# Optimization experiments

Hardware: AMD Instinct MI355X
Metric: run time of the kernel (lower is better)

Reference implementation:

```python
import jax, jax.numpy as jnp
import numpy as np

B, N = 4, 2048
K_GLOBAL, K_LOCAL = 32, 16
EMB, OUT_C = 1024, 40
NEG, EPS = 0.2, 1e-5


def _bn(x, p, axis=1):
    # p: (4, C) stacked (gamma, beta, running_mean, running_var); eval-mode BN
    g, b, m, v = p
    sh = [1] * x.ndim
    sh[axis] = -1
    return (x - m.reshape(sh)) * (g.reshape(sh) * jax.lax.rsqrt(v.reshape(sh) + EPS)) + b.reshape(sh)


def _knn(geod, allow, k):
    # geod: (B,N,N) affinity (larger = closer, as in DGCNN's -dist^2 convention)
    # allow: (B,N) bool columns that may be selected
    mn = jnp.min(geod, axis=-1, keepdims=True)           # (B,N,1) row minima
    pd = jnp.where(allow[:, None, :], geod, mn)          # disallowed cols -> row min (never picked)
    return jax.lax.top_k(pd, k)[1]                       # (B,N,k)


def _edge_conv(x, geod, allow, k, w, bnp):
    # x: (B,C,N); EdgeConv: gather neighbors, cat(nbr-ctr, ctr), 1x1 conv, BN, LeakyReLU, max over k
    idx = _knn(geod, allow, k)                           # (B,N,k)
    xt = jnp.swapaxes(x, 1, 2)                           # (B,N,C)
    nbr = jax.vmap(lambda a, i: a[i])(xt, idx)           # (B,N,k,C)
    ctr = xt[:, :, None, :]
    feat = jnp.concatenate([nbr - ctr, jnp.broadcast_to(ctr, nbr.shape)], axis=-1)  # (B,N,k,2C)
    y = jnp.einsum('oc,bnkc->bonk', w, feat)             # 1x1 conv (no bias)
    y = jax.nn.leaky_relu(_bn(y, bnp, 1), NEG)
    return jnp.max(y, axis=-1)                           # (B,O,N)


def setup_inputs() -> dict:
    key = jax.random.key(0)
    ks = list(jax.random.split(key, 64))
    it = iter(ks)
    d = {}
    d['x'] = jax.random.normal(next(it), (B, 3, N), jnp.float32)
    d['local_idx'] = jax.random.randint(next(it), (B, N), 0, 2).astype(bool)
    d['geod_dist'] = jax.random.normal(next(it), (B, N, N), jnp.float32)
    dims = [(64, 6), (64, 128), (128, 128), (256, 256), (64, 6), (64, 128), (128, 128), (256, 256), (EMB, 512)]
    for i, (o, c) in enumerate(dims, 1):
        d[f'w{i}'] = (jax.random.normal(next(it), (o, c), jnp.float32) / np.sqrt(c)).astype(jnp.float32)
    bn_c = [64, 64, 128, 256, 64, 64, 128, 256, EMB, 512, 256]
    for i, c in enumerate(bn_c, 1):
        g = 1.0 + 0.05 * jax.random.normal(next(it), (c,))
        b = 0.05 * jax.random.normal(next(it), (c,))
        m = 0.05 * jax.random.normal(next(it), (c,))
        v = jax.random.uniform(next(it), (c,), minval=0.5, maxval=1.5)
        d[f'bn{i}'] = jnp.stack([g, b, m, v]).astype(jnp.float32)
    d['lin1_w'] = (jax.random.normal(next(it), (512, 2 * EMB)) / np.sqrt(2 * EMB)).astype(jnp.float32)
    d['lin2_w'] = (jax.random.normal(next(it), (256, 512)) / np.sqrt(512)).astype(jnp.float32)
    d['lin2_b'] = (0.01 * jax.random.normal(next(it), (256,))).astype(jnp.float32)
    d['lin3_w'] = (jax.random.normal(next(it), (OUT_C, 256)) / np.sqrt(256)).astype(jnp.float32)
    d['lin3_b'] = (0.01 * jax.random.normal(next(it), (OUT_C,))).astype(jnp.float32)
    return d


def reference(x, local_idx, geod_dist, w1, w2, w3, w4, w5, w6, w7, w8, w9,
              bn1, bn2, bn3, bn4, bn5, bn6, bn7, bn8, bn9, bn10, bn11,
              lin1_w, lin2_w, lin2_b, lin3_w, lin3_b):
    allow_l = local_idx          # local branch: neighbors restricted to local points
    allow_g = ~local_idx         # global branch: neighbors restricted to non-local points
    # local branch (kl neighbors)
    xl1 = _edge_conv(x, geod_dist, allow_l, K_LOCAL, w1, bn1)
    xl2 = _edge_conv(xl1, geod_dist, allow_l, K_LOCAL, w2, bn2)
    xl3 = _edge_conv(xl2, geod_dist, allow_l, K_LOCAL, w3, bn3)
    xl4 = _edge_conv(xl3, geod_dist, allow_l, K_LOCAL, w4, bn4)
    x_local = jnp.concatenate([xl1, xl2, xl3, xl4], axis=1)   # (B,512,N)
    # global branch (k neighbors)
    xg1 = _edge_conv(x, geod_dist, allow_g, K_GLOBAL, w5, bn5)
    xg2 = _edge_conv(xg1, geod_dist, allow_g, K_GLOBAL, w6, bn6)
    xg3 = _edge_conv(xg2, geod_dist, allow_g, K_GLOBAL, w7, bn7)
    xg4 = _edge_conv(xg3, geod_dist, allow_g, K_GLOBAL, w8, bn8)
    x_glob = jnp.concatenate([xg1, xg2, xg3, xg4], axis=1)    # (B,512,N)
    # overwrite local points' features with local-branch features
    xm = jnp.where(local_idx[:, None, :], x_local, x_glob)
    y = jnp.einsum('oc,bcn->bon', w9, xm)                     # conv9 1x1
    y = jax.nn.leaky_relu(_bn(y, bn9, 1), NEG)                # (B,EMB,N)
    p = jnp.concatenate([jnp.max(y, axis=-1), jnp.mean(y, axis=-1)], axis=1)  # (B,2*EMB)
    h = jax.nn.leaky_relu(_bn(p @ lin1_w.T, bn10, 1), NEG)
    h = jax.nn.leaky_relu(_bn(h @ lin2_w.T + lin2_b, bn11, 1), NEG)
    return h @ lin3_w.T + lin3_b                              # (B,OUT_C)
```

## Files before the change

### kernel.cpp

```cpp
#include <hip/hip_runtime.h>
#include <stdint.h>

#define NPTS 2048
#define NB 4
#define NROWS (NB * NPTS)
#define LNEG 0.2f

typedef unsigned long long u64;

static __device__ __forceinline__ uint32_t sortable_f32(float f) {
  uint32_t u = __float_as_uint(f);
  return u ^ ((u >> 31) ? 0xFFFFFFFFu : 0x80000000u);
}

static __device__ __forceinline__ float lrelu(float t) { return t >= 0.f ? t : LNEG * t; }

__global__ void detect_mode_k(const uint32_t* __restrict__ loc, int* __restrict__ mode) {
  __shared__ uint32_t mAll, mOdd;
  if (threadIdx.x == 0) { mAll = 0u; mOdd = 0u; }
  __syncthreads();
  uint32_t a = 0u, o = 0u;
  for (int i = threadIdx.x; i < 2048; i += 256) {
    uint32_t v = loc[i];
    a = a > v ? a : v;
    if (i & 1) o = o > v ? o : v;
  }
  atomicMax(&mAll, a);
  atomicMax(&mOdd, o);
  __syncthreads();
  if (threadIdx.x == 0) {
    int m;
    if (mAll > 1u) m = 0;
    else if (mOdd == 0u) m = 2;
    else m = 1;
    *mode = m;
  }
}

__device__ __forceinline__ bool read_allow(const void* loc, int mode, int i) {
  if (mode == 0) return ((const uint8_t*)loc)[i] != 0;
  if (mode == 1) return ((const int*)loc)[i] != 0;
  return ((const uint32_t*)loc)[(size_t)i * 2] != 0;
}

struct PrepArgs {
  const float* x; float* x0;
  const float* w[9]; float* wt[9];
  int O[9], C[9];
  const float* bn[11]; float* bns[11]; float* bnb[11];
  int bc[11];
};

__global__ void prep_k(PrepArgs pa) {
  int idx = blockIdx.x * 256 + threadIdx.x;
  if (idx < NROWS * 3) {
    int c = idx % 3, r = idx / 3;
    int b = r >> 11, n = r & (NPTS - 1);
    pa.x0[idx] = pa.x[((size_t)b * 3 + c) * NPTS + n];
    return;
  }
  idx -= NROWS * 3;
  #pragma unroll
  for (int l = 0; l < 9; ++l) {
    int O = pa.O[l], C = pa.C[l];
    int n2 = (l == 8) ? O : 2 * O;
    int sz = C * n2;
    if (idx < sz) {
      int o = idx % n2, c = idx / n2;
      float v;
      if (l == 8) v = pa.w[l][(size_t)o * C + c];
      else if (o < O) v = pa.w[l][(size_t)o * 2 * C + c];
      else v = pa.w[l][(size_t)(o - O) * 2 * C + C + c]
             - pa.w[l][(size_t)(o - O) * 2 * C + c];
      pa.wt[l][(size_t)c * n2 + o] = v;
      return;
    }
    idx -= sz;
  }
  #pragma unroll
  for (int i = 0; i < 11; ++i) {
    int C = pa.bc[i];
    if (idx < C) {
      float g = pa.bn[i][idx], b = pa.bn[i][C + idx];
      float m = pa.bn[i][2 * C + idx], v = pa.bn[i][3 * C + idx];
      float s = g * rsqrtf(v + 1e-5f);
      pa.bns[i][idx] = s;
      pa.bnb[i][idx] = b - m * s;
      return;
    }
    idx -= C;
  }
}

__global__ __launch_bounds__(256) void knn_k(const float* __restrict__ geod,
                                             const void* __restrict__ loc,
                                             const int* __restrict__ modep,
                                             int* __restrict__ idxL,
                                             int* __restrict__ idxG) {
  int row = blockIdx.x;
  int b = row >> 11;
  int tid = threadIdx.x;
  int wid = tid >> 6, lane = tid & 63;
  int mode = *modep;
  const float* g = geod + (size_t)row * NPTS;

  float v[8];
  uint32_t amask = 0;
  float lmin = INFINITY;
  #pragma unroll
  for (int e = 0; e < 8; ++e) {
    int j = tid + 256 * e;
    v[e] = g[j];
    if (read_allow(loc, mode, b * NPTS + j)) amask |= (1u << e);
    lmin = fminf(lmin, v[e]);
  }
  __shared__ float sred[4];
  #pragma unroll
  for (int off = 32; off; off >>= 1) lmin = fminf(lmin, __shfl_xor(lmin, off));
  if (lane == 0) sred[wid] = lmin;
  __syncthreads();
  lmin = fminf(fminf(sred[0], sred[1]), fminf(sred[2], sred[3]));
  uint32_t smin = sortable_f32(lmin);

  __shared__ u64 skey[2][4];

  auto runsel = [&](u64 (&key)[8], int K, int* outp) {
    u64 tmax = key[0];
    #pragma unroll
    for (int e = 1; e < 8; ++e) tmax = tmax > key[e] ? tmax : key[e];
    {
      u64 m = tmax;
      #pragma unroll
      for (int off = 32; off; off >>= 1) {
        unsigned lo = __shfl_xor((unsigned)m, off);
        unsigned hi = __shfl_xor((unsigned)(m >> 32), off);
        u64 om = ((u64)hi << 32) | lo;
        m = m > om ? m : om;
      }
      if (lane == 0) skey[0][wid] = m;
    }
    __syncthreads();
    u64 wm0 = skey[0][0], wm1 = skey[0][1], wm2 = skey[0][2], wm3 = skey[0][3];
    int wprev = 0;
    for (int it = 0; it < K; ++it) {
      if (it) {
        u64 nv = skey[(it - 1) & 1][wprev];
        wm0 = (wprev == 0) ? nv : wm0;
        wm1 = (wprev == 1) ? nv : wm1;
        wm2 = (wprev == 2) ? nv : wm2;
        wm3 = (wprev == 3) ? nv : wm3;
      }
      u64 M = wm0; int ws = 0;
      if (wm1 > M) { M = wm1; ws = 1; }
      if (wm2 > M) { M = wm2; ws = 2; }
      if (wm3 > M) { M = wm3; ws = 3; }
      int j = (NPTS - 1) - (int)(M & (u64)(NPTS - 1));
      if (tid == 0) outp[it] = j;
      if (wid == ws) {
        if ((j & 255) == tid) {
          int e = j >> 8;
          #pragma unroll
          for (int t = 0; t < 8; ++t) key[t] = (t == e) ? 0ull : key[t];
          tmax = key[0];
          #pragma unroll
          for (int t = 1; t < 8; ++t) tmax = tmax > key[t] ? tmax : key[t];
        }
        u64 m = tmax;
        #pragma unroll
        for (int off = 32; off; off >>= 1) {
          unsigned lo = __shfl_xor((unsigned)m, off);
          unsigned hi = __shfl_xor((unsigned)(m >> 32), off);
          u64 om = ((u64)hi << 32) | lo;
          m = m > om ? m : om;
        }
        if (lane == 0) skey[it & 1][ws] = m;
      }
      wprev = ws;
      __syncthreads();
    }
  };

  {
    u64 keyL[8];
    #pragma unroll
    for (int e = 0; e < 8; ++e) {
      int j = tid + 256 * e;
      uint32_t sv = sortable_f32(v[e]);
      uint32_t kl = (amask >> e & 1u) ? sv : smin;
      keyL[e] = ((u64)kl << 11) | (unsigned)(NPTS - 1 - j);
    }
    runsel(keyL, 16, idxL + (size_t)row * 16);
  }
  {
    u64 keyG[8];
    #pragma unroll
    for (int e = 0; e < 8; ++e) {
      int j = tid + 256 * e;
      uint32_t sv = sortable_f32(v[e]);
      uint32_t kg = (amask >> e & 1u) ? smin : sv;
      keyG[e] = ((u64)kg << 11) | (unsigned)(NPTS - 1 - j);
    }
    runsel(keyG, 32, idxG + (size_t)row * 32);
  }
}

#define BM 64
#define BNC 64
#define BKC 16

__global__ __launch_bounds__(256) void gemm_k(const float* __restrict__ A, int lda,
                                              const float* __restrict__ Bt, int K, int N2,
                                              float* __restrict__ C, int ldc,
                                              const float* __restrict__ sc,
                                              const float* __restrict__ bi, int act) {
  __shared__ float As[BKC][BM + 4];
  __shared__ float Bs[BKC][BNC + 4];
  int tid = threadIdx.x;
  int tx = tid & 15, ty = tid >> 4;
  int m0 = blockIdx.x * BM, n0 = blockIdx.y * BNC;
  float acc[4][4] = {};
  for (int k0 = 0; k0 < K; k0 += BKC) {
    #pragma unroll
    for (int i = tid; i < BM * BKC; i += 256) {
      int kk = i & 15, mm = i >> 4;
      int kg = k0 + kk;
      As[kk][mm] = (kg < K) ? A[(size_t)(m0 + mm) * lda + kg] : 0.f;
    }
    #pragma unroll
    for (int i = tid; i < BKC * BNC; i += 256) {
      int nn = i & 63, kk = i >> 6;
      int kg = k0 + kk;
      Bs[kk][nn] = (kg < K) ? Bt[(size_t)kg * N2 + n0 + nn] : 0.f;
    }
    __syncthreads();
    #pragma unroll
    for (int k = 0; k < BKC; ++k) {
      float4 a4 = *(const float4*)&As[k][tx * 4];
      float4 b4 = *(const float4*)&Bs[k][ty * 4];
      float a[4] = {a4.x, a4.y, a4.z, a4.w};
      float bb[4] = {b4.x, b4.y, b4.z, b4.w};
      #pragma unroll
      for (int i2 = 0; i2 < 4; ++i2)
        #pragma unroll
        for (int j2 = 0; j2 < 4; ++j2)
          acc[i2][j2] = fmaf(a[i2], bb[j2], acc[i2][j2]);
    }
    __syncthreads();
  }
  #pragma unroll
  for (int i2 = 0; i2 < 4; ++i2) {
    int m = m0 + tx * 4 + i2;
    float4 o4;
    float* ov = (float*)&o4;
    #pragma unroll
    for (int j2 = 0; j2 < 4; ++j2) {
      int n = n0 + ty * 4 + j2;
      float vv = acc[i2][j2];
      if (act) {
        vv = fmaf(vv, sc[n], bi[n]);
        vv = lrelu(vv);
      }
      ov[j2] = vv;
    }
    *(float4*)&C[(size_t)m * ldc + n0 + ty * 4] = o4;
  }
}

#define GBM 128
#define GBN 64
#define GBK 16

__global__ __launch_bounds__(256) void gemmbig_k(const float* __restrict__ A, int lda,
                                                 const float* __restrict__ Bt, int K, int N2,
                                                 float* __restrict__ C, int ldc,
                                                 const float* __restrict__ sc,
                                                 const float* __restrict__ bi, int act) {
  __shared__ float As[2][GBK][GBM + 4];
  __shared__ float Bs[2][GBK][GBN + 4];
  int tid = threadIdx.x;
  int tx = tid & 15, ty = tid >> 4;
  int m0 = blockIdx.x * GBM, n0 = blockIdx.y * GBN;
  int ar = tid >> 2;
  int ak = (tid & 3) * 4;
  int bk = tid >> 4;
  int bn = (tid & 15) * 4;
  const int nk = K / GBK;
  float4 a0, a1, b0;
  auto load_tile = [&](int kt) {
    int k0 = kt * GBK;
    a0 = *(const float4*)&A[(size_t)(m0 + ar) * lda + k0 + ak];
    a1 = *(const float4*)&A[(size_t)(m0 + 64 + ar) * lda + k0 + ak];
    b0 = *(const float4*)&Bt[(size_t)(k0 + bk) * N2 + n0 + bn];
  };
  auto store_tile = [&](int buf) {
    As[buf][ak + 0][ar] = a0.x; As[buf][ak + 1][ar] = a0.y;
    As[buf][ak + 2][ar] = a0.z; As[buf][ak + 3][ar] = a0.w;
    As[buf][ak + 0][64 + ar] = a1.x; As[buf][ak + 1][64 + ar] = a1.y;
    As[buf][ak + 2][64 + ar] = a1.z; As[buf][ak + 3][64 + ar] = a1.w;
    *(float4*)&Bs[buf][bk][bn] = b0;
  };
  float acc[2][4][4] = {};
  load_tile(0);
  store_tile(0);
  __syncthreads();
  for (int kt = 0; kt < nk; ++kt) {
    int cur = kt & 1;
    if (kt + 1 < nk) load_tile(kt + 1);
    #pragma unroll
    for (int k = 0; k < GBK; ++k) {
      float a[2][4], b[4];
      *(float4*)a[0] = *(const float4*)&As[cur][k][tx * 4];
      *(float4*)a[1] = *(const float4*)&As[cur][k][64 + tx * 4];
      *(float4*)b = *(const float4*)&Bs[cur][k][ty * 4];
      #pragma unroll
      for (int im = 0; im < 2; ++im)
        #pragma unroll
        for (int i = 0; i < 4; ++i)
          #pragma unroll
          for (int j = 0; j < 4; ++j)
            acc[im][i][j] = fmaf(a[im][i], b[j], acc[im][i][j]);
    }
    if (kt + 1 < nk) store_tile(1 - cur);
    __syncthreads();
  }
  #pragma unroll
  for (int im = 0; im < 2; ++im)
    #pragma unroll
    for (int i = 0; i < 4; ++i) {
      int m = m0 + im * 64 + tx * 4 + i;
      int nbase = n0 + ty * 4;
      float4 o4;
      float* ov = (float*)&o4;
      #pragma unroll
      for (int j = 0; j < 4; ++j) {
        float vv = acc[im][i][j];
        if (act) {
          vv = fmaf(vv, sc[nbase + j], bi[nbase + j]);
          vv = lrelu(vv);
        }
        ov[j] = vv;
      }
      *(float4*)&C[(size_t)m * ldc + nbase] = o4;
    }
}

template<int K, int O>
__global__ __launch_bounds__(256) void gather_k(const float* __restrict__ z,
                                                const int* __restrict__ idx,
                                                const float* __restrict__ scale,
                                                const float* __restrict__ bias,
                                                float* __restrict__ outp) {
  constexpr int LDZ = 2 * O;
  int wid = threadIdx.x >> 6, lane = threadIdx.x & 63;
  int point = (blockIdx.x << 2) + wid;
  int b = point >> 11;
  const int* ip = idx + (size_t)point * K;
  int jj[K];
  #pragma unroll
  for (int k = 0; k < K; ++k) jj[k] = ip[k];
  if constexpr (O >= 256) {
    int c = lane * 4;
    float4 mx = {-INFINITY, -INFINITY, -INFINITY, -INFINITY};
    float4 mn = {INFINITY, INFINITY, INFINITY, INFINITY};
    #pragma unroll
    for (int k = 0; k < K; ++k) {
      float4 v = *(const float4*)&z[(size_t)((b << 11) + jj[k]) * LDZ + c];
      mx.x = fmaxf(mx.x, v.x); mx.y = fmaxf(mx.y, v.y);
      mx.z = fmaxf(mx.z, v.z); mx.w = fmaxf(mx.w, v.w);
      mn.x = fminf(mn.x, v.x); mn.y = fminf(mn.y, v.y);
      mn.z = fminf(mn.z, v.z); mn.w = fminf(mn.w, v.w);
    }
    float4 zc = *(const float4*)&z[(size_t)point * LDZ + O + c];
    float4 s = *(const float4*)&scale[c];
    float4 bb = *(const float4*)&bias[c];
    float4 o;
    o.x = lrelu(fmaf((s.x >= 0.f ? mx.x : mn.x) + zc.x, s.x, bb.x));
    o.y = lrelu(fmaf((s.y >= 0.f ? mx.y : mn.y) + zc.y, s.y, bb.y));
    o.z = lrelu(fmaf((s.z >= 0.f ? mx.z : mn.z) + zc.z, s.z, bb.z));
    o.w = lrelu(fmaf((s.w >= 0.f ? mx.w : mn.w) + zc.w, s.w, bb.w));
    *(float4*)&outp[(size_t)point * 512 + c] = o;
  } else if constexpr (O == 128) {
    int c = lane * 2;
    float2 mx = {-INFINITY, -INFINITY}, mn = {INFINITY, INFINITY};
    #pragma unroll
    for (int k = 0; k < K; ++k) {
      float2 v = *(const float2*)&z[(size_t)((b << 11) + jj[k]) * LDZ + c];
      mx.x = fmaxf(mx.x, v.x); mx.y = fmaxf(mx.y, v.y);
      mn.x = fminf(mn.x, v.x); mn.y = fminf(mn.y, v.y);
    }
    float2 zc = *(const float2*)&z[(size_t)point * LDZ + O + c];
    float2 s = *(const float2*)&scale[c];
    float2 bb = *(const float2*)&bias[c];
    float2 o;
    o.x = lrelu(fmaf((s.x >= 0.f ? mx.x : mn.x) + zc.x, s.x, bb.x));
    o.y = lrelu(fmaf((s.y >= 0.f ? mx.y : mn.y) + zc.y, s.y, bb.y));
    *(float2*)&outp[(size_t)point * 512 + c] = o;
  } else {
    int c = lane;
    float mx = -INFINITY, mn = INFINITY;
    #pragma unroll
    for (int k = 0; k < K; ++k) {
      float v = z[(size_t)((b << 11) + jj[k]) * LDZ + c];
      mx = fmaxf(mx, v);
      mn = fminf(mn, v);
    }
    float zc = z[(size_t)point * LDZ + O + c];
    float s = scale[c], bb = bias[c];
    float t = fmaf((s >= 0.f ? mx : mn) + zc, s, bb);
    outp[(size_t)point * 512 + c] = lrelu(t);
  }
}

__global__ __launch_bounds__(256) void select_k(const float* __restrict__ xl,
                                                const float* __restrict__ xg,
                                                const void* __restrict__ loc,
                                                const int* __restrict__ modep,
                                                float* __restrict__ xm) {
  int i = blockIdx.x * 256 + threadIdx.x;
  int row = i >> 7;
  int mode = *modep;
  bool l = read_allow(loc, mode, row);
  const float4* s = (const float4*)(l ? xl : xg);
  ((float4*)xm)[i] = s[i];
}

__global__ __launch_bounds__(256) void reduce_np_k(const float* __restrict__ y,
                                                   float* __restrict__ p) {
  int b = blockIdx.x >> 4, cb = blockIdx.x & 15;
  int wid = threadIdx.x >> 6, lane = threadIdx.x & 63;
  int c = cb * 64 + lane;
  float mx = -INFINITY, sm = 0.f;
  for (int n = wid; n < NPTS; n += 4) {
    float v = y[((size_t)(b * NPTS + n)) * 1024 + c];
    mx = fmaxf(mx, v);
    sm += v;
  }
  __shared__ float smx[4][64], ssm[4][64];
  smx[wid][lane] = mx;
  ssm[wid][lane] = sm;
  __syncthreads();
  if (wid == 0) {
    #pragma unroll
    for (int w = 1; w < 4; ++w) { mx = fmaxf(mx, smx[w][lane]); sm += ssm[w][lane]; }
    p[b * 2048 + c] = mx;
    p[b * 2048 + 1024 + c] = sm * (1.f / 2048.f);
  }
}

__global__ __launch_bounds__(256) void mlp1_k(const float* __restrict__ p,
                                              const float* __restrict__ w,
                                              const float* __restrict__ s10,
                                              const float* __restrict__ b10,
                                              float* __restrict__ h1) {
  int o = (blockIdx.x << 2) + (threadIdx.x >> 6);
  int lane = threadIdx.x & 63;
  const float4* wr = (const float4*)(w + (size_t)o * 2048);
  float acc[NB] = {};
  for (int i = lane; i < 512; i += 64) {
    float4 wv = wr[i];
    #pragma unroll
    for (int b = 0; b < NB; ++b) {
      float4 pv = ((const float4*)(p + b * 2048))[i];
      acc[b] += wv.x * pv.x + wv.y * pv.y + wv.z * pv.z + wv.w * pv.w;
    }
  }
  #pragma unroll
  for (int off = 32; off; off >>= 1)
    #pragma unroll
    for (int b = 0; b < NB; ++b) acc[b] += __shfl_xor(acc[b], off);
  if (lane == 0) {
    float sc = s10[o], bc = b10[o];
    #pragma unroll
    for (int b = 0; b < NB; ++b) h1[b * 512 + o] = lrelu(fmaf(acc[b], sc, bc));
  }
}

__global__ __launch_bounds__(256) void mlp2_k(const float* __restrict__ h1,
                                              const float* __restrict__ w,
                                              const float* __restrict__ l2b,
                                              const float* __restrict__ s11,
                                              const float* __restrict__ b11,
                                              float* __restrict__ h2) {
  int o = (blockIdx.x << 2) + (threadIdx.x >> 6);
  int lane = threadIdx.x & 63;
  const float4* wr = (const float4*)(w + (size_t)o * 512);
  float acc[NB] = {};
  for (int i = lane; i < 128; i += 64) {
    float4 wv = wr[i];
    #pragma unroll
    for (int b = 0; b < NB; ++b) {
      float4 pv = ((const float4*)(h1 + b * 512))[i];
      acc[b] += wv.x * pv.x + wv.y * pv.y + wv.z * pv.z + wv.w * pv.w;
    }
  }
  #pragma unroll
  for (int off = 32; off; off >>= 1)
    #pragma unroll
    for (int b = 0; b < NB; ++b) acc[b] += __shfl_xor(acc[b], off);
  if (lane == 0) {
    float bl = l2b[o], sc = s11[o], bc = b11[o];
    #pragma unroll
    for (int b = 0; b < NB; ++b) h2[b * 256 + o] = lrelu(fmaf(acc[b] + bl, sc, bc));
  }
}

__global__ __launch_bounds__(256) void mlp3_k(const float* __restrict__ h2,
                                              const float* __restrict__ w,
                                              const float* __restrict__ l3b,
                                              float* __restrict__ outp) {
  int o = (blockIdx.x << 2) + (threadIdx.x >> 6);
  int lane = threadIdx.x & 63;
  if (o >= 40) return;
  const float4* wr = (const float4*)(w + (size_t)o * 256);
  float acc[NB] = {};
  for (int i = lane; i < 64; i += 64) {
    float4 wv = wr[i];
    #pragma unroll
    for (int b = 0; b < NB; ++b) {
      float4 pv = ((const float4*)(h2 + b * 256))[i];
      acc[b] += wv.x * pv.x + wv.y * pv.y + wv.z * pv.z + wv.w * pv.w;
    }
  }
  #pragma unroll
  for (int off = 32; off; off >>= 1)
    #pragma unroll
    for (int b = 0; b < NB; ++b) acc[b] += __shfl_xor(acc[b], off);
  if (lane == 0) {
    float bl = l3b[o];
    #pragma unroll
    for (int b = 0; b < NB; ++b) outp[b * 40 + o] = acc[b] + bl;
  }
}

extern "C" void kernel_launch(void* const* d_in, const int* in_sizes, int n_in,
                              void* d_out, int out_size, void* d_ws, size_t ws_size,
                              hipStream_t stream) {
  const float* x = (const float*)d_in[0];
  const void* loc = d_in[1];
  const float* geod = (const float*)d_in[2];
  const float* w[9];
  for (int i = 0; i < 9; ++i) w[i] = (const float*)d_in[3 + i];
  const float* bn[11];
  for (int i = 0; i < 11; ++i) bn[i] = (const float*)d_in[12 + i];
  const float* l1w = (const float*)d_in[23];
  const float* l2w = (const float*)d_in[24];
  const float* l2b = (const float*)d_in[25];
  const float* l3w = (const float*)d_in[26];
  const float* l3b = (const float*)d_in[27];
  float* outp = (float*)d_out;

  char* base = (char*)d_ws;
  size_t off = 0;
  auto alloc = [&](size_t bytes) -> void* {
    void* p = base + off;
    off += (bytes + 255) & ~(size_t)255;
    return p;
  };
  int* mode = (int*)alloc(4);
  float* x0 = (float*)alloc((size_t)NROWS * 3 * 4);
  int* idxL = (int*)alloc((size_t)NROWS * 16 * 4);
  int* idxG = (int*)alloc((size_t)NROWS * 32 * 4);
  static const int Oc[9] = {64, 64, 128, 256, 64, 64, 128, 256, 1024};
  static const int Cc[9] = {3, 64, 64, 128, 3, 64, 64, 128, 512};
  float* wt[9];
  for (int l = 0; l < 9; ++l) {
    int n2 = (l == 8) ? Oc[l] : 2 * Oc[l];
    wt[l] = (float*)alloc((size_t)Cc[l] * n2 * 4);
  }
  static const int bc[11] = {64, 64, 128, 256, 64, 64, 128, 256, 1024, 512, 256};
  float *bns[11], *bnb[11];
  for (int i = 0; i < 11; ++i) {
    bns[i] = (float*)alloc((size_t)bc[i] * 4);
    bnb[i] = (float*)alloc((size_t)bc[i] * 4);
  }
  float* z = (float*)alloc((size_t)NROWS * 1024 * 4);
  float* xcatL = (float*)alloc((size_t)NROWS * 512 * 4);
  float* xcatG = (float*)alloc((size_t)NROWS * 512 * 4);
  float* xm = (float*)alloc((size_t)NROWS * 512 * 4);
  float* pbuf = (float*)alloc((size_t)NB * 2048 * 4);
  float* h1 = (float*)alloc((size_t)NB * 512 * 4);
  float* h2 = (float*)alloc((size_t)NB * 256 * 4);

  detect_mode_k<<<1, 256, 0, stream>>>((const uint32_t*)loc, mode);

  PrepArgs pa;
  pa.x = x; pa.x0 = x0;
  for (int l = 0; l < 9; ++l) { pa.w[l] = w[l]; pa.wt[l] = wt[l]; pa.O[l] = Oc[l]; pa.C[l] = Cc[l]; }
  for (int i = 0; i < 11; ++i) { pa.bn[i] = bn[i]; pa.bns[i] = bns[i]; pa.bnb[i] = bnb[i]; pa.bc[i] = bc[i]; }
  int total = NROWS * 3;
  for (int l = 0; l < 9; ++l) total += Cc[l] * ((l == 8) ? Oc[l] : 2 * Oc[l]);
  for (int i = 0; i < 11; ++i) total += bc[i];
  prep_k<<<(total + 255) / 256, 256, 0, stream>>>(pa);

  knn_k<<<NROWS, 256, 0, stream>>>(geod, loc, mode, idxL, idxG);

  auto gemm = [&](const float* A, int lda, const float* Bt, int K, int N2, float* C, int ldc,
                  const float* sc, const float* bi, int act) {
    if (N2 >= 512) {
      dim3 grid(NROWS / GBM, N2 / GBN);
      gemmbig_k<<<grid, 256, 0, stream>>>(A, lda, Bt, K, N2, C, ldc, sc, bi, act);
    } else {
      dim3 grid(NROWS / BM, N2 / BNC);
      gemm_k<<<grid, 256, 0, stream>>>(A, lda, Bt, K, N2, C, ldc, sc, bi, act);
    }
  };
  auto gather = [&](int K, int O, const int* idx, const float* sc, const float* bi, float* op) {
    dim3 grid(NROWS / 4);
    if (K == 16) {
      if (O == 64)       gather_k<16, 64><<<grid, 256, 0, stream>>>(z, idx, sc, bi, op);
      else if (O == 128) gather_k<16, 128><<<grid, 256, 0, stream>>>(z, idx, sc, bi, op);
      else               gather_k<16, 256><<<grid, 256, 0, stream>>>(z, idx, sc, bi, op);
    } else {
      if (O == 64)       gather_k<32, 64><<<grid, 256, 0, stream>>>(z, idx, sc, bi, op);
      else if (O == 128) gather_k<32, 128><<<grid, 256, 0, stream>>>(z, idx, sc, bi, op);
      else               gather_k<32, 256><<<grid, 256, 0, stream>>>(z, idx, sc, bi, op);
    }
  };

  static const int coff[4] = {0, 64, 128, 256};
  for (int l = 0; l < 4; ++l) {
    const float* A = (l == 0) ? x0 : (xcatL + coff[l - 1]);
    int lda = (l == 0) ? 3 : 512;
    gemm(A, lda, wt[l], Cc[l], 2 * Oc[l], z, 2 * Oc[l], nullptr, nullptr, 0);
    gather(16, Oc[l], idxL, bns[l], bnb[l], xcatL + coff[l]);
  }
  for (int l = 0; l < 4; ++l) {
    const float* A = (l == 0) ? x0 : (xcatG + coff[l - 1]);
    int lda = (l == 0) ? 3 : 512;
    gemm(A, lda, wt[4 + l], Cc[4 + l], 2 * Oc[4 + l], z, 2 * Oc[4 + l], nullptr, nullptr, 0);
    gather(32, Oc[4 + l], idxG, bns[4 + l], bnb[4 + l], xcatG + coff[l]);
  }

  select_k<<<(NROWS * 512 / 4) / 256, 256, 0, stream>>>(xcatL, xcatG, loc, mode, xm);
  gemm(xm, 512, wt[8], 512, 1024, z, 1024, bns[8], bnb[8], 1);
  reduce_np_k<<<NB * 16, 256, 0, stream>>>(z, pbuf);
  mlp1_k<<<128, 256, 0, stream>>>(pbuf, l1w, bns[9], bnb[9], h1);
  mlp2_k<<<64, 256, 0, stream>>>(h1, l2w, l2b, bns[10], bnb[10], h2);
  mlp3_k<<<10, 256, 0, stream>>>(h2, l3w, l3b, outp);
}
```

Baseline: 859.0 us.

## Run each kNN selection within a single wavefront instead of a block

The top-k selection kernel now assigns one wavefront per (row, local/global) task, so each block covers two rows and no longer splits a row across four waves. This removes the per-iteration __syncthreads and shared-memory exchange of wave maxima during the iterative argmax. Each lane holds 32 keys in registers, which raises register pressure. The geodesic row is read twice per task (once for the minimum, once to build keys) and is also read by both the local and global tasks of the same row.

```diff
diff --git a/kernel.cpp b/kernel.cpp
--- a/kernel.cpp
+++ b/kernel.cpp
@@ -97,110 +97,57 @@
                                              const int* __restrict__ modep,
                                              int* __restrict__ idxL,
                                              int* __restrict__ idxG) {
-  int row = blockIdx.x;
+  int wid = threadIdx.x >> 6, lane = threadIdx.x & 63;
+  int task = (blockIdx.x << 2) + wid;
+  int row = task >> 1;
+  bool isG = task & 1;
   int b = row >> 11;
-  int tid = threadIdx.x;
-  int wid = tid >> 6, lane = tid & 63;
   int mode = *modep;
   const float* g = geod + (size_t)row * NPTS;
 
-  float v[8];
-  uint32_t amask = 0;
   float lmin = INFINITY;
   #pragma unroll
-  for (int e = 0; e < 8; ++e) {
-    int j = tid + 256 * e;
-    v[e] = g[j];
-    if (read_allow(loc, mode, b * NPTS + j)) amask |= (1u << e);
-    lmin = fminf(lmin, v[e]);
-  }
-  __shared__ float sred[4];
+  for (int e = 0; e < 32; ++e) lmin = fminf(lmin, g[lane + 64 * e]);
   #pragma unroll
   for (int off = 32; off; off >>= 1) lmin = fminf(lmin, __shfl_xor(lmin, off));
-  if (lane == 0) sred[wid] = lmin;
-  __syncthreads();
-  lmin = fminf(fminf(sred[0], sred[1]), fminf(sred[2], sred[3]));
   uint32_t smin = sortable_f32(lmin);
 
-  __shared__ u64 skey[2][4];
-
-  auto runsel = [&](u64 (&key)[8], int K, int* outp) {
-    u64 tmax = key[0];
-    #pragma unroll
-    for (int e = 1; e < 8; ++e) tmax = tmax > key[e] ? tmax : key[e];
-    {
-      u64 m = tmax;
+  u64 key[32];
+  #pragma unroll
+  for (int e = 0; e < 32; ++e) {
+    int j = lane + 64 * e;
+    bool allow = read_allow(loc, mode, b * NPTS + j);
+    if (isG) allow = !allow;
+    uint32_t kv = allow ? sortable_f32(g[j]) : smin;
+    key[e] = ((u64)kv << 11) | (unsigned)(NPTS - 1 - j);
+  }
+  u64 tmax = key[0];
+  #pragma unroll
+  for (int e = 1; e < 32; ++e) tmax = tmax > key[e] ? tmax : key[e];
+
+  int K = isG ? 32 : 16;
+  int* outp = isG ? (idxG + (size_t)row * 32) : (idxL + (size_t)row * 16);
+  for (int it = 0; it < K; ++it) {
+    u64 m = tmax;
+    #pragma unroll
+    for (int off = 32; off; off >>= 1) {
+      unsigned lo = __shfl_xor((unsigned)m, off);
+      unsigned hi = __shfl_xor((unsigned)(m >> 32), off);
+      u64 om = ((u64)hi << 32) | lo;
+      m = m > om ? m : om;
+    }
+    int j = (NPTS - 1) - (int)(m & (u64)(NPTS - 1));
+    if (lane == 0) outp[it] = j;
+    if (lane == (j & 63)) {
+      int e = j >> 6;
+      u64 nm = 0;
       #pragma unroll
-      for (int off = 32; off; off >>= 1) {
-        unsigned lo = __shfl_xor((unsigned)m, off);
-        unsigned hi = __shfl_xor((unsigned)(m >> 32), off);
-        u64 om = ((u64)hi << 32) | lo;
-        m = m > om ? m : om;
+      for (int t = 0; t < 32; ++t) {
+        key[t] = (t == e) ? 0ull : key[t];
+        nm = nm > key[t] ? nm : key[t];
       }
-      if (lane == 0) skey[0][wid] = m;
-    }
-    __syncthreads();
-    u64 wm0 = skey[0][0], wm1 = skey[0][1], wm2 = skey[0][2], wm3 = skey[0][3];
-    int wprev = 0;
-    for (int it = 0; it < K; ++it) {
-      if (it) {
-        u64 nv = skey[(it - 1) & 1][wprev];
-        wm0 = (wprev == 0) ? nv : wm0;
-        wm1 = (wprev == 1) ? nv : wm1;
-        wm2 = (wprev == 2) ? nv : wm2;
-        wm3 = (wprev == 3) ? nv : wm3;
-      }
-      u64 M = wm0; int ws = 0;
-      if (wm1 > M) { M = wm1; ws = 1; }
-      if (wm2 > M) { M = wm2; ws = 2; }
-      if (wm3 > M) { M = wm3; ws = 3; }
-      int j = (NPTS - 1) - (int)(M & (u64)(NPTS - 1));
-      if (tid == 0) outp[it] = j;
-      if (wid == ws) {
-        if ((j & 255) == tid) {
-          int e = j >> 8;
-          #pragma unroll
-          for (int t = 0; t < 8; ++t) key[t] = (t == e) ? 0ull : key[t];
-          tmax = key[0];
-          #pragma unroll
-          for (int t = 1; t < 8; ++t) tmax = tmax > key[t] ? tmax : key[t];
-        }
-        u64 m = tmax;
-        #pragma unroll
-        for (int off = 32; off; off >>= 1) {
-          unsigned lo = __shfl_xor((unsigned)m, off);
-          unsigned hi = __shfl_xor((unsigned)(m >> 32), off);
-          u64 om = ((u64)hi << 32) | lo;
-          m = m > om ? m : om;
-        }
-        if (lane == 0) skey[it & 1][ws] = m;
-      }
-      wprev = ws;
-      __syncthreads();
-    }
-  };
-
-  {
-    u64 keyL[8];
-    #pragma unroll
-    for (int e = 0; e < 8; ++e) {
-      int j = tid + 256 * e;
-      uint32_t sv = sortable_f32(v[e]);
-      uint32_t kl = (amask >> e & 1u) ? sv : smin;
-      keyL[e] = ((u64)kl << 11) | (unsigned)(NPTS - 1 - j);
-    }
-    runsel(keyL, 16, idxL + (size_t)row * 16);
-  }
-  {
-    u64 keyG[8];
-    #pragma unroll
-    for (int e = 0; e < 8; ++e) {
-      int j = tid + 256 * e;
-      uint32_t sv = sortable_f32(v[e]);
-      uint32_t kg = (amask >> e & 1u) ? smin : sv;
-      keyG[e] = ((u64)kg << 11) | (unsigned)(NPTS - 1 - j);
-    }
-    runsel(keyG, 32, idxG + (size_t)row * 32);
+      tmax = nm;
+    }
   }
 }
 
@@ -592,7 +539,7 @@
   for (int i = 0; i < 11; ++i) total += bc[i];
   prep_k<<<(total + 255) / 256, 256, 0, stream>>>(pa);
 
-  knn_k<<<NROWS, 256, 0, stream>>>(geod, loc, mode, idxL, idxG);
+  knn_k<<<NROWS / 2, 256, 0, stream>>>(geod, loc, mode, idxL, idxG);
 
   auto gemm = [&](const float* A, int lda, const float* Bt, int K, int N2, float* C, int ldc,
                   const float* sc, const float* bi, int act) {
```

After: 851.5 us. About the same (-0.9%).
